# Kernel tuning notes

Measured on AMD Instinct MI355X. Metric: run time of the kernel, lower is better.

## Reference

```python
import jax, jax.numpy as jnp
from jax import lax
import numpy as np

DN = ('NHWC', 'HWIO', 'NHWC')  # NHWC activations, HWIO kernels (TF layout)
EPS = 1e-3


def setup_inputs() -> dict:
    key = jax.random.key(0)
    ks = jax.random.split(key, 6)
    B, H, W, C = 16, 64, 64, 256
    x = jax.random.normal(ks[0], (B, H, W, C), jnp.float32)
    # per-sample predicted kernels (scaled to keep activations well-conditioned)
    depthwise_kernels = jax.random.normal(ks[1], (B, 3, 3, C, C), jnp.float32) * 0.02
    pointwise_kernels = jax.random.normal(ks[2], (B, 1, 1, C, C), jnp.float32) * 0.06
    biases = jax.random.normal(ks[3], (B, C), jnp.float32) * 0.1
    # shared trailing Conv2D layer params
    conv_w = jax.random.normal(ks[4], (3, 3, C, C), jnp.float32) * 0.02
    conv_b = jnp.zeros((C,), jnp.float32)
    return dict(x=x, depthwise_kernels=depthwise_kernels,
                pointwise_kernels=pointwise_kernels, biases=biases,
                conv_w=conv_w, conv_b=conv_b)


def _instance_norm(x):
    # tf.nn.moments over spatial dims (population variance), eps=0.001
    mean = jnp.mean(x, axis=(1, 2), keepdims=True)
    var = jnp.var(x, axis=(1, 2), keepdims=True)
    return (x - mean) * lax.rsqrt(var + EPS)


def _reflect_pad_hw(x, p=1):
    pad = [(0, 0)] * (x.ndim - 3) + [(p, p), (p, p), (0, 0)]
    return jnp.pad(x, pad, mode='reflect')


def _per_sample_conv(xi, dk, pk, bi):
    # xi: [H,W,C]; dk: [3,3,C,Cm]; pk: [1,1,Cm,Co]; bi: [Co]
    xp = _reflect_pad_hw(xi)[None]  # [1,H+2,W+2,C]
    y = lax.conv_general_dilated(xp, dk, (1, 1), 'VALID', dimension_numbers=DN)
    y = lax.conv_general_dilated(y, pk, (1, 1), 'VALID', dimension_numbers=DN)
    return (y + bi)[0]


def reference(x, depthwise_kernels, pointwise_kernels, biases, conv_w, conv_b):
    x = _instance_norm(x)
    # per-sample kernels -> vmap over batch (replaces tf.map_fn)
    x = jax.vmap(_per_sample_conv)(x, depthwise_kernels, pointwise_kernels, biases)
    # shared Conv2D: reflect pad + VALID conv + bias
    xp = _reflect_pad_hw(x)
    y = lax.conv_general_dilated(xp, conv_w, (1, 1), 'VALID', dimension_numbers=DN)
    return y + conv_b
```

## Files before the change

kernel.cpp:

```cpp
#include <hip/hip_runtime.h>


typedef __bf16 bf16x8 __attribute__((ext_vector_type(8)));
typedef float f32x4 __attribute__((ext_vector_type(4)));

__device__ __forceinline__ float bf2f(unsigned short v) {
    return __uint_as_float(((unsigned int)v) << 16);
}
__device__ __forceinline__ unsigned short f2bf(float f) {
    unsigned int u = __float_as_uint(f);
    unsigned int r = (u + 0x7FFFu + ((u >> 16) & 1u)) >> 16;
    return (unsigned short)r;
}
__device__ __forceinline__ float ldg_elem(const void* p, size_t idx, bool isbf) {
    return isbf ? bf2f(((const unsigned short*)p)[idx]) : ((const float*)p)[idx];
}

__device__ __forceinline__ void gload16(const void* g, void* l) {
    __builtin_amdgcn_global_load_lds(
        (__attribute__((address_space(1))) void*)(unsigned long long)g,
        (__attribute__((address_space(3))) void*)(unsigned long long)l,
        16, 0, 0);
}

__global__ void detect_dtype(const unsigned short* __restrict__ x, int* __restrict__ flag) {
    __shared__ int wild;
    if (threadIdx.x == 0) wild = 0;
    __syncthreads();
    int cnt = 0;
    for (int i = 0; i < 16; ++i) {
        float a = fabsf(bf2f(x[threadIdx.x * 16 + i]));
        if (!(a < 64.f) || (a != 0.f && a < 1e-5f)) cnt++;
    }
    atomicAdd(&wild, cnt);
    __syncthreads();
    if (threadIdx.x == 0) *flag = (wild > 512) ? 0 : 1;
}


__global__ void init_stats(float* s) { s[blockIdx.x * 256 + threadIdx.x] = 0.f; }

__global__ void norm_partial(const void* __restrict__ x, const int* __restrict__ flag,
                             float* __restrict__ ssum, float* __restrict__ ssq) {
    const bool isbf = (*flag != 0);
    const int b = blockIdx.x, chunk = blockIdx.y, c = threadIdx.x;
    const size_t base = ((size_t)(b * 4096 + chunk * 64)) * 256 + c;
    float s = 0.f, q = 0.f;
    for (int i = 0; i < 64; ++i) {
        float v = ldg_elem(x, base + (size_t)i * 256, isbf);
        s += v; q += v * v;
    }
    atomicAdd(&ssum[b * 256 + c], s);
    atomicAdd(&ssq[b * 256 + c], q);
}

__global__ void norm_finalize(float* ssum, float* ssq) {
    int i = blockIdx.x * 256 + threadIdx.x;
    float mean = ssum[i] * (1.f / 4096.f);
    float var  = ssq[i]  * (1.f / 4096.f) - mean * mean;
    ssum[i] = mean;
    ssq[i]  = rsqrtf(var + 1e-3f);
}

__global__ void norm_apply(const void* __restrict__ x, const int* __restrict__ flag,
                           const float* __restrict__ mean, const float* __restrict__ rstd,
                           unsigned short* __restrict__ xn) {
    const bool isbf = (*flag != 0);
    size_t e = ((size_t)blockIdx.x * 256 + threadIdx.x) * 8;
    int c0 = (int)(e & 255);
    int bc = (int)(e >> 20) * 256 + c0;
    float v[8];
    if (isbf) {
        uint4 raw = *(const uint4*)((const unsigned short*)x + e);
        unsigned int rr[4] = {raw.x, raw.y, raw.z, raw.w};
#pragma unroll
        for (int i = 0; i < 4; ++i) {
            v[2 * i]     = bf2f((unsigned short)(rr[i] & 0xFFFF));
            v[2 * i + 1] = bf2f((unsigned short)(rr[i] >> 16));
        }
    } else {
        float4 f0 = *(const float4*)((const float*)x + e);
        float4 f1 = *(const float4*)((const float*)x + e + 4);
        v[0] = f0.x; v[1] = f0.y; v[2] = f0.z; v[3] = f0.w;
        v[4] = f1.x; v[5] = f1.y; v[6] = f1.z; v[7] = f1.w;
    }
    unsigned int o[4];
#pragma unroll
    for (int i = 0; i < 4; ++i) {
        unsigned short lo = f2bf((v[2 * i]     - mean[bc + 2 * i])     * rstd[bc + 2 * i]);
        unsigned short hi = f2bf((v[2 * i + 1] - mean[bc + 2 * i + 1]) * rstd[bc + 2 * i + 1]);
        o[i] = (unsigned int)lo | ((unsigned int)hi << 16);
    }
    uint4 out; out.x = o[0]; out.y = o[1]; out.z = o[2]; out.w = o[3];
    *(uint4*)(xn + e) = out;
}

template <bool SCALE>
__global__ void transpose_wk(const void* __restrict__ src, const int* __restrict__ flag,
                             unsigned short* __restrict__ dst,
                             int s_per, long dstBStride, int coStride,
                             const float* __restrict__ rstd) {
    __shared__ unsigned short tile[64][66];
    const bool isbf = (*flag != 0);
    const int sl = blockIdx.x;
    const int b = sl / s_per;
    const size_t dbase = (size_t)b * (size_t)dstBStride + (size_t)(sl % s_per) * 256;
    const int ci0 = blockIdx.y * 64, co0 = blockIdx.z * 64;
    const int t = threadIdx.x;
    const int co4 = (t & 15) * 4;
    const int r0 = t >> 4;
#pragma unroll
    for (int i = 0; i < 4; ++i) {
        int r = r0 + i * 16;
        size_t sidx = (size_t)sl * 65536 + (size_t)(ci0 + r) * 256 + co0 + co4;
        if (isbf) {
            ushort4 v = *(const ushort4*)((const unsigned short*)src + sidx);
            tile[r][co4] = v.x; tile[r][co4 + 1] = v.y;
            tile[r][co4 + 2] = v.z; tile[r][co4 + 3] = v.w;
        } else {
            float4 v = *(const float4*)((const float*)src + sidx);
            tile[r][co4] = f2bf(v.x); tile[r][co4 + 1] = f2bf(v.y);
            tile[r][co4 + 2] = f2bf(v.z); tile[r][co4 + 3] = f2bf(v.w);
        }
    }
    __syncthreads();
    const int cip = (t & 31) * 2;
    const int cob = t >> 5;
    float s0 = 1.f, s1 = 1.f;
    if (SCALE) { s0 = rstd[b * 256 + ci0 + cip]; s1 = rstd[b * 256 + ci0 + cip + 1]; }
#pragma unroll
    for (int i = 0; i < 8; ++i) {
        int co = cob + i * 8;
        unsigned short lo = tile[cip][co], hi = tile[cip + 1][co];
        if (SCALE) { lo = f2bf(bf2f(lo) * s0); hi = f2bf(bf2f(hi) * s1); }
        *(unsigned int*)(dst + dbase + (size_t)(co0 + co) * coStride + ci0 + cip) =
            (unsigned int)lo | ((unsigned int)hi << 16);
    }
}

__global__ void corr_kernel(const unsigned short* __restrict__ dkT,
                            const float* __restrict__ mean,
                            float* __restrict__ negcorr) {
    const int b = blockIdx.x;
    const int lane = threadIdx.x & 63;
    const int co = blockIdx.y * 4 + (threadIdx.x >> 6);
    const unsigned short* wp = dkT + (size_t)(b * 256 + co) * 2304;
    const float* mb = mean + b * 256;
    const int ci0 = (lane & 31) * 8;
    float4 ma = *(const float4*)(mb + ci0);
    float4 mc = *(const float4*)(mb + ci0 + 4);
    float mm[8] = {ma.x, ma.y, ma.z, ma.w, mc.x, mc.y, mc.z, mc.w};
    float sum = 0.f;
#pragma unroll
    for (int c = 0; c < 5; ++c) {
        int k = c * 512 + lane * 8;
        if (k < 2304) {
            uint4 w = *(const uint4*)(wp + k);
            unsigned int wsv[4] = {w.x, w.y, w.z, w.w};
#pragma unroll
            for (int j = 0; j < 4; ++j) {
                sum += bf2f((unsigned short)(wsv[j] & 0xFFFF)) * mm[2 * j];
                sum += bf2f((unsigned short)(wsv[j] >> 16)) * mm[2 * j + 1];
            }
        }
    }
#pragma unroll
    for (int off = 32; off > 0; off >>= 1) sum += __shfl_down(sum, off);
    if (lane == 0) negcorr[b * 256 + co] = -sum;
}

template <int KSLICES, bool PER_SAMPLE_W, int BIAS_MODE, bool IS3X3, bool OUT_F32>
__global__ __launch_bounds__(256) void gemm_conv_dma(const unsigned short* __restrict__ src,
                                                     const int* __restrict__ flag,
                                                     const unsigned short* __restrict__ wT,
                                                     const void* __restrict__ bias,
                                                     void* __restrict__ dst) {
    constexpr int KTOT = KSLICES * 256;
    __shared__ unsigned short As[128 * 64];
    __shared__ unsigned short Bs[128 * 64];

    const int t = threadIdx.x;
    const int lane = t & 63;
    const int wave = t >> 6;
    const int b = blockIdx.z;
    const int m0 = blockIdx.x * 128;
    const int n0 = blockIdx.y * 128;
    const unsigned short* srcB = src + (size_t)b * (4096 * 256);
    const unsigned short* wB = wT + (PER_SAMPLE_W ? (size_t)b * 256 * KTOT : (size_t)0);
    const bool in_bf = (BIAS_MODE >= 2) ? (*flag != 0) : true;

    f32x4 acc[4][4];
#pragma unroll
    for (int i = 0; i < 4; ++i)
#pragma unroll
        for (int j = 0; j < 4; ++j) acc[i][j] = (f32x4){0.f, 0.f, 0.f, 0.f};

    const int lr = lane >> 3;
    const int cidx = lane & 7;
    const int swz = ((cidx ^ lr) << 3);

    int hA[4], wA[4];
    const unsigned short* gB[4];
    unsigned short* ldsA[4];
    unsigned short* ldsB[4];
#pragma unroll
    for (int c = 0; c < 4; ++c) {
        int r = wave * 32 + c * 8;
        int m = m0 + r + lr;
        hA[c] = m >> 6; wA[c] = m & 63;
        gB[c] = wB + (size_t)(n0 + r + lr) * KTOT + swz;
        ldsA[c] = As + r * 64;
        ldsB[c] = Bs + r * 64;
    }

    const int fr = lane & 15;
    const int quad = lane >> 4;
    const int rm = (wave >> 1) * 64;
    const int cn = (wave & 1) * 64;
    const int fsw = fr & 7;

    for (int s = 0; s < KSLICES; ++s) {
        const int dh = IS3X3 ? (s / 3) - 1 : 0;
        const int dw = IS3X3 ? (s % 3) - 1 : 0;
        const unsigned short* gA[4];
#pragma unroll
        for (int c = 0; c < 4; ++c) {
            int hh = hA[c] + dh; hh = (hh < 0) ? 1 : (hh > 63 ? 62 : hh);
            int ww = wA[c] + dw; ww = (ww < 0) ? 1 : (ww > 63 ? 62 : ww);
            gA[c] = srcB + (size_t)((hh << 6) + ww) * 256 + swz;
        }
        const int kbase = s * 256;
#pragma unroll
        for (int cc = 0; cc < 4; ++cc) {
            __syncthreads();
#pragma unroll
            for (int c = 0; c < 4; ++c) {
                gload16(gA[c] + cc * 64, ldsA[c]);
                gload16(gB[c] + kbase + cc * 64, ldsB[c]);
            }
            __syncthreads();

#pragma unroll
            for (int step = 0; step < 2; ++step) {
                const int ks = ((quad + step * 4) ^ fsw) << 3;
                bf16x8 af[4], bfr[4];
#pragma unroll
                for (int i = 0; i < 4; ++i)
                    af[i] = *(const bf16x8*)&As[(rm + i * 16 + fr) * 64 + ks];
#pragma unroll
                for (int j = 0; j < 4; ++j)
                    bfr[j] = *(const bf16x8*)&Bs[(cn + j * 16 + fr) * 64 + ks];
#pragma unroll
                for (int i = 0; i < 4; ++i)
#pragma unroll
                    for (int j = 0; j < 4; ++j)
                        acc[i][j] = __builtin_amdgcn_mfma_f32_16x16x32_bf16(af[i], bfr[j], acc[i][j], 0, 0, 0);
            }
        }
    }

    const int rbase = quad * 4;
    const int col = fr;
    float bv[4];
#pragma unroll
    for (int j = 0; j < 4; ++j) {
        int n = n0 + cn + j * 16 + col;
        if (BIAS_MODE == 2)      bv[j] = ldg_elem(bias, b * 256 + n, in_bf);
        else if (BIAS_MODE == 3) bv[j] = ldg_elem(bias, n, in_bf);
        else                     bv[j] = 0.f;
    }
#pragma unroll
    for (int i = 0; i < 4; ++i) {
#pragma unroll
        for (int rr = 0; rr < 4; ++rr) {
            int m = m0 + rm + i * 16 + rbase + rr;
            size_t rowoff = ((size_t)b * 4096 + m) * 256;
#pragma unroll
            for (int j = 0; j < 4; ++j) {
                int n = n0 + cn + j * 16 + col;
                float val = acc[i][j][rr] + bv[j];
                if (OUT_F32) ((float*)dst)[rowoff + n] = val;
                else         ((unsigned short*)dst)[rowoff + n] = f2bf(val);
            }
        }
    }
}

template <int KSLICES, bool PER_SAMPLE_W, int BIAS_MODE, bool IS3X3, bool SRC_ADAPT, bool OUT_F32>
__global__ __launch_bounds__(256) void gemm_conv(const void* __restrict__ src,
                                                 const int* __restrict__ flag,
                                                 const unsigned short* __restrict__ wT,
                                                 const void* __restrict__ bias,
                                                 void* __restrict__ dst) {
    constexpr int KTOT = KSLICES * 256;
    __shared__ unsigned short As[128][40];
    __shared__ unsigned short Bs[128][40];

    const bool in_bf = (SRC_ADAPT || BIAS_MODE >= 2) ? (*flag != 0) : true;
    const int t = threadIdx.x;
    const int b = blockIdx.z;
    const int m0 = blockIdx.x * 128;
    const int n0 = blockIdx.y * 128;
    const size_t srcOfs = (size_t)b * (4096 * 256);
    const unsigned short* wB = wT + (PER_SAMPLE_W ? (size_t)b * 256 * KTOT : (size_t)0);

    f32x4 acc[4][4];
#pragma unroll
    for (int i = 0; i < 4; ++i)
#pragma unroll
        for (int j = 0; j < 4; ++j) acc[i][j] = (f32x4){0.f, 0.f, 0.f, 0.f};

    const int lane = t & 63;
    const int wave = t >> 6;
    const int rm = (wave >> 1) * 64;
    const int cn = (wave & 1) * 64;
    const int fr = lane & 15;
    const int kg = (lane >> 4) * 8;

    for (int kk = 0; kk < KTOT / 32; ++kk) {
        const int k0 = kk * 32;
        const int s = k0 >> 8;
        const int ci0 = k0 & 255;
        const int dh = IS3X3 ? (s / 3) - 1 : 0;
        const int dw = IS3X3 ? (s % 3) - 1 : 0;
        __syncthreads();
#pragma unroll
        for (int cc = 0; cc < 2; ++cc) {
            int ch = t + cc * 256;
            int r = ch >> 2;
            int ko = (ch & 3) << 3;
            int m = m0 + r;
            int h = m >> 6, w = m & 63;
            if (IS3X3) {
                h += dh; h = (h < 0) ? 1 : (h > 63 ? 62 : h);
                w += dw; w = (w < 0) ? 1 : (w > 63 ? 62 : w);
            }
            size_t eidx = srcOfs + (size_t)((h << 6) + w) * 256 + ci0 + ko;
            if (!SRC_ADAPT || in_bf) {
                uint4 v = *(const uint4*)((const unsigned short*)src + eidx);
                *(uint4*)&As[r][ko] = v;
            } else {
                const float* sf = (const float*)src + eidx;
                float4 f0 = *(const float4*)sf;
                float4 f1 = *(const float4*)(sf + 4);
                uint4 v;
                v.x = (unsigned int)f2bf(f0.x) | ((unsigned int)f2bf(f0.y) << 16);
                v.y = (unsigned int)f2bf(f0.z) | ((unsigned int)f2bf(f0.w) << 16);
                v.z = (unsigned int)f2bf(f1.x) | ((unsigned int)f2bf(f1.y) << 16);
                v.w = (unsigned int)f2bf(f1.z) | ((unsigned int)f2bf(f1.w) << 16);
                *(uint4*)&As[r][ko] = v;
            }
        }
#pragma unroll
        for (int cc = 0; cc < 2; ++cc) {
            int ch = t + cc * 256;
            int n = ch >> 2;
            int ko = (ch & 3) << 3;
            uint4 v = *(const uint4*)(wB + (size_t)(n0 + n) * KTOT + k0 + ko);
            *(uint4*)&Bs[n][ko] = v;
        }
        __syncthreads();

        bf16x8 af[4], bfr[4];
#pragma unroll
        for (int i = 0; i < 4; ++i) af[i] = *(const bf16x8*)&As[rm + i * 16 + fr][kg];
#pragma unroll
        for (int j = 0; j < 4; ++j) bfr[j] = *(const bf16x8*)&Bs[cn + j * 16 + fr][kg];
#pragma unroll
        for (int i = 0; i < 4; ++i)
#pragma unroll
            for (int j = 0; j < 4; ++j)
                acc[i][j] = __builtin_amdgcn_mfma_f32_16x16x32_bf16(af[i], bfr[j], acc[i][j], 0, 0, 0);
    }

    const int rbase = (lane >> 4) * 4;
    const int col = lane & 15;
    float bv[4];
#pragma unroll
    for (int j = 0; j < 4; ++j) {
        int n = n0 + cn + j * 16 + col;
        if (BIAS_MODE == 1)      bv[j] = ((const float*)bias)[b * 256 + n];
        else if (BIAS_MODE == 2) bv[j] = ldg_elem(bias, b * 256 + n, in_bf);
        else if (BIAS_MODE == 3) bv[j] = ldg_elem(bias, n, in_bf);
        else                     bv[j] = 0.f;
    }
#pragma unroll
    for (int i = 0; i < 4; ++i) {
#pragma unroll
        for (int rr = 0; rr < 4; ++rr) {
            int m = m0 + rm + i * 16 + rbase + rr;
            size_t rowoff = ((size_t)b * 4096 + m) * 256;
#pragma unroll
            for (int j = 0; j < 4; ++j) {
                int n = n0 + cn + j * 16 + col;
                float val = acc[i][j][rr] + bv[j];
                if (OUT_F32) ((float*)dst)[rowoff + n] = val;
                else         ((unsigned short*)dst)[rowoff + n] = f2bf(val);
            }
        }
    }
}

extern "C" void kernel_launch(void* const* d_in, const int* in_sizes, int n_in,
                              void* d_out, int out_size, void* d_ws, size_t ws_size,
                              hipStream_t stream) {
    const void* x    = d_in[0];
    const void* dk   = d_in[1];
    const void* pk   = d_in[2];
    const void* bias = d_in[3];
    const void* cw   = d_in[4];
    const void* cb   = d_in[5];

    const size_t NEED_SMALL = 36896768u;
    const size_t NEED_BIG   = 55771136u;
    if (ws_size < NEED_SMALL) return;
    const bool big = (ws_size >= NEED_BIG);

    char* ws = (char*)d_ws;
    int*   flagp   = (int*)ws;
    float* meanp   = (float*)(ws + 1024);
    float* rstdp   = (float*)(ws + 17408);
    float* negcorr = (float*)(ws + 33792);
    unsigned short* pkT = (unsigned short*)(ws + 65536);
    unsigned short* cwT = (unsigned short*)(ws + 2162688);
    unsigned short* dkT = (unsigned short*)(ws + 3342336);
    unsigned short* xn  = (unsigned short*)(ws + 22216704);
    unsigned short* y2  = big ? xn : dkT;
    unsigned short* y1  = (unsigned short*)d_out;

    detect_dtype<<<1, 256, 0, stream>>>((const unsigned short*)x, flagp);
    init_stats<<<32, 256, 0, stream>>>(meanp);
    norm_partial<<<dim3(16, 64), 256, 0, stream>>>(x, flagp, meanp, rstdp);
    norm_finalize<<<16, 256, 0, stream>>>(meanp, rstdp);

    transpose_wk<false><<<dim3(16, 4, 4), 256, 0, stream>>>(pk, flagp, pkT, 1, 65536L, 256, nullptr);
    transpose_wk<false><<<dim3(9, 4, 4), 256, 0, stream>>>(cw, flagp, cwT, 9, 0L, 2304, nullptr);

    if (big) {
        transpose_wk<false><<<dim3(144, 4, 4), 256, 0, stream>>>(dk, flagp, dkT, 9, 589824L, 2304, nullptr);
        norm_apply<<<8192, 256, 0, stream>>>(x, flagp, meanp, rstdp, xn);
        gemm_conv_dma<9, true, 0, true, false><<<dim3(32, 2, 16), 256, 0, stream>>>(xn, flagp, dkT, nullptr, y1);
    } else {
        transpose_wk<true><<<dim3(144, 4, 4), 256, 0, stream>>>(dk, flagp, dkT, 9, 589824L, 2304, rstdp);
        corr_kernel<<<dim3(16, 64), 256, 0, stream>>>(dkT, meanp, negcorr);
        gemm_conv<9, true, 1, true, true, false><<<dim3(32, 2, 16), 256, 0, stream>>>(x, flagp, dkT, negcorr, y1);
    }

    gemm_conv_dma<1, true, 2, false, false><<<dim3(32, 2, 16), 256, 0, stream>>>(y1, flagp, pkT, bias, y2);
    gemm_conv_dma<9, false, 3, true, true><<<dim3(32, 2, 16), 256, 0, stream>>>(y2, flagp, cwT, cb, d_out);
}
```

Before: 390.1 us.

## Add 256x256-tile 512-thread pipelined GEMM for the 3x3 convolutions

```diff
diff --git a/kernel.cpp b/kernel.cpp
--- a/kernel.cpp
+++ b/kernel.cpp
@@ -22,6 +22,10 @@
         (__attribute__((address_space(3))) void*)(unsigned long long)l,
         16, 0, 0);
 }
+
+#define RAW_BARRIER() do { asm volatile("" ::: "memory"); \
+                           __builtin_amdgcn_s_barrier();   \
+                           asm volatile("" ::: "memory"); } while (0)
 
 __global__ void detect_dtype(const unsigned short* __restrict__ x, int* __restrict__ flag) {
     __shared__ int wild;
@@ -170,6 +174,204 @@
 }
 
 template <int KSLICES, bool PER_SAMPLE_W, int BIAS_MODE, bool IS3X3, bool OUT_F32>
+__global__ __launch_bounds__(512, 2) void gemm_conv_256(const unsigned short* __restrict__ src,
+                                                        const int* __restrict__ flag,
+                                                        const unsigned short* __restrict__ wT,
+                                                        const void* __restrict__ bias,
+                                                        void* __restrict__ dst) {
+    constexpr int KTOT = KSLICES * 256;
+    constexpr int NKT = KTOT / 64;
+    static_assert(NKT >= 2, "pipeline needs >=2 K-tiles");
+    extern __shared__ unsigned short smem[];
+
+    const int t = threadIdx.x;
+    const int lane = t & 63;
+    const int wave = t >> 6;
+    const int wr = wave >> 2;
+    const int wc = wave & 3;
+    const int b = blockIdx.z;
+    const int m0 = blockIdx.x * 256;
+    const unsigned short* srcB = src + (size_t)b * (4096 * 256);
+    const unsigned short* wB = wT + (PER_SAMPLE_W ? (size_t)b * 256 * KTOT : (size_t)0);
+    const bool in_bf = (BIAS_MODE >= 2) ? (*flag != 0) : true;
+
+    const int trow = t >> 3;
+    const int tswz = ((t & 7) ^ (trow & 7)) << 3;
+    int hU[4], wU[4];
+#pragma unroll
+    for (int u = 0; u < 4; ++u) {
+        int m = m0 + u * 64 + trow;
+        hU[u] = m >> 6; wU[u] = m & 63;
+    }
+    const unsigned short* gBu[4];
+#pragma unroll
+    for (int u = 0; u < 4; ++u)
+        gBu[u] = wB + (size_t)(u * 64 + trow) * KTOT + tswz;
+
+    f32x4 acc[8][4];
+#pragma unroll
+    for (int i = 0; i < 8; ++i)
+#pragma unroll
+        for (int j = 0; j < 4; ++j) acc[i][j] = (f32x4){0.f, 0.f, 0.f, 0.f};
+
+    const int fr = lane & 15;
+    const int quad = lane >> 4;
+    const int fsw = fr & 7;
+    const int ks0 = ((quad) ^ fsw) << 3;
+    const int ks1 = ((quad + 4) ^ fsw) << 3;
+    const int rm = wr * 128;
+    const int cn = wc * 64;
+
+#pragma unroll
+    for (int kt = 0; kt < 2; ++kt) {
+        const int s0_ = kt >> 2;
+        const int pdh = IS3X3 ? (s0_ / 3) - 1 : 0;
+        const int pdw = IS3X3 ? (s0_ % 3) - 1 : 0;
+        const int pchb = (kt & 3) << 6;
+        unsigned short* ldsAW = smem + kt * 32768 + wave * 512;
+#pragma unroll
+        for (int u = 0; u < 4; ++u) {
+            int hh = hU[u] + pdh; hh = (hh < 0) ? 1 : (hh > 63 ? 62 : hh);
+            int ww = wU[u] + pdw; ww = (ww < 0) ? 1 : (ww > 63 ? 62 : ww);
+            gload16(srcB + (size_t)((hh << 6) + ww) * 256 + pchb + tswz, ldsAW + u * 4096);
+        }
+#pragma unroll
+        for (int u = 0; u < 4; ++u)
+            gload16(gBu[u] + (size_t)kt * 64, ldsAW + 16384 + u * 4096);
+    }
+    asm volatile("s_waitcnt vmcnt(8)" ::: "memory");
+    RAW_BARRIER();
+
+    bf16x8 af[4][2], bfr[4][2];
+
+    for (int i = 0; i < NKT; ++i) {
+        const int buf = i & 1;
+        const unsigned short* As_b = smem + buf * 32768;
+        const unsigned short* Bs_b = As_b + 16384;
+        unsigned short* ldsAW = smem + buf * 32768 + wave * 512;
+        const int kt2 = i + 2;
+        const bool st = (kt2 < NKT);
+        int dh2 = 0, dw2 = 0, chb2 = 0;
+        if (st) {
+            int s2 = kt2 >> 2;
+            dh2 = IS3X3 ? (s2 / 3) - 1 : 0;
+            dw2 = IS3X3 ? (s2 % 3) - 1 : 0;
+            chb2 = (kt2 & 3) << 6;
+        }
+        auto stA = [&](int u) {
+            int hh = hU[u] + dh2; hh = (hh < 0) ? 1 : (hh > 63 ? 62 : hh);
+            int ww = wU[u] + dw2; ww = (ww < 0) ? 1 : (ww > 63 ? 62 : ww);
+            gload16(srcB + (size_t)((hh << 6) + ww) * 256 + chb2 + tswz, ldsAW + u * 4096);
+        };
+        auto stB = [&](int u) {
+            gload16(gBu[u] + (size_t)kt2 * 64, ldsAW + 16384 + u * 4096);
+        };
+
+#pragma unroll
+        for (int m = 0; m < 4; ++m) {
+            const unsigned short* rp = As_b + (rm + m * 16 + fr) * 64;
+            af[m][0] = *(const bf16x8*)(rp + ks0);
+            af[m][1] = *(const bf16x8*)(rp + ks1);
+        }
+#pragma unroll
+        for (int n = 0; n < 2; ++n) {
+            const unsigned short* rp = Bs_b + (cn + n * 16 + fr) * 64;
+            bfr[n][0] = *(const bf16x8*)(rp + ks0);
+            bfr[n][1] = *(const bf16x8*)(rp + ks1);
+        }
+        RAW_BARRIER();
+        __builtin_amdgcn_s_setprio(1);
+#pragma unroll
+        for (int m = 0; m < 4; ++m)
+#pragma unroll
+            for (int n = 0; n < 2; ++n) {
+                acc[m][n] = __builtin_amdgcn_mfma_f32_16x16x32_bf16(af[m][0], bfr[n][0], acc[m][n], 0, 0, 0);
+                acc[m][n] = __builtin_amdgcn_mfma_f32_16x16x32_bf16(af[m][1], bfr[n][1], acc[m][n], 0, 0, 0);
+            }
+        __builtin_amdgcn_s_setprio(0);
+        RAW_BARRIER();
+
+#pragma unroll
+        for (int n = 2; n < 4; ++n) {
+            const unsigned short* rp = Bs_b + (cn + n * 16 + fr) * 64;
+            bfr[n][0] = *(const bf16x8*)(rp + ks0);
+            bfr[n][1] = *(const bf16x8*)(rp + ks1);
+        }
+        if (st) { stA(0); stA(2); }
+        RAW_BARRIER();
+        __builtin_amdgcn_s_setprio(1);
+#pragma unroll
+        for (int m = 0; m < 4; ++m)
+#pragma unroll
+            for (int n = 2; n < 4; ++n) {
+                acc[m][n] = __builtin_amdgcn_mfma_f32_16x16x32_bf16(af[m][0], bfr[n][0], acc[m][n], 0, 0, 0);
+                acc[m][n] = __builtin_amdgcn_mfma_f32_16x16x32_bf16(af[m][1], bfr[n][1], acc[m][n], 0, 0, 0);
+            }
+        __builtin_amdgcn_s_setprio(0);
+        RAW_BARRIER();
+
+#pragma unroll
+        for (int m = 0; m < 4; ++m) {
+            const unsigned short* rp = As_b + (rm + 64 + m * 16 + fr) * 64;
+            af[m][0] = *(const bf16x8*)(rp + ks0);
+            af[m][1] = *(const bf16x8*)(rp + ks1);
+        }
+        if (st) { stB(0); stB(1); }
+        RAW_BARRIER();
+        __builtin_amdgcn_s_setprio(1);
+#pragma unroll
+        for (int m = 0; m < 4; ++m)
+#pragma unroll
+            for (int n = 0; n < 2; ++n) {
+                acc[4 + m][n] = __builtin_amdgcn_mfma_f32_16x16x32_bf16(af[m][0], bfr[n][0], acc[4 + m][n], 0, 0, 0);
+                acc[4 + m][n] = __builtin_amdgcn_mfma_f32_16x16x32_bf16(af[m][1], bfr[n][1], acc[4 + m][n], 0, 0, 0);
+            }
+        __builtin_amdgcn_s_setprio(0);
+        RAW_BARRIER();
+
+        if (st) { stB(2); stB(3); stA(1); stA(3); }
+        RAW_BARRIER();
+        __builtin_amdgcn_s_setprio(1);
+#pragma unroll
+        for (int m = 0; m < 4; ++m)
+#pragma unroll
+            for (int n = 2; n < 4; ++n) {
+                acc[4 + m][n] = __builtin_amdgcn_mfma_f32_16x16x32_bf16(af[m][0], bfr[n][0], acc[4 + m][n], 0, 0, 0);
+                acc[4 + m][n] = __builtin_amdgcn_mfma_f32_16x16x32_bf16(af[m][1], bfr[n][1], acc[4 + m][n], 0, 0, 0);
+            }
+        __builtin_amdgcn_s_setprio(0);
+        if (st)                  asm volatile("s_waitcnt vmcnt(8)" ::: "memory");
+        else if (i + 1 < NKT)    asm volatile("s_waitcnt vmcnt(0)" ::: "memory");
+        RAW_BARRIER();
+    }
+
+    const int rbase = quad * 4;
+    float bv[4];
+#pragma unroll
+    for (int n = 0; n < 4; ++n) {
+        int nn = cn + n * 16 + fr;
+        if (BIAS_MODE == 2)      bv[n] = ldg_elem(bias, b * 256 + nn, in_bf);
+        else if (BIAS_MODE == 3) bv[n] = ldg_elem(bias, nn, in_bf);
+        else                     bv[n] = 0.f;
+    }
+#pragma unroll
+    for (int m = 0; m < 8; ++m) {
+#pragma unroll
+        for (int rr = 0; rr < 4; ++rr) {
+            int mm = m0 + rm + m * 16 + rbase + rr;
+            size_t rowoff = ((size_t)b * 4096 + mm) * 256;
+#pragma unroll
+            for (int n = 0; n < 4; ++n) {
+                int nn = cn + n * 16 + fr;
+                float val = acc[m][n][rr] + bv[n];
+                if (OUT_F32) ((float*)dst)[rowoff + nn] = val;
+                else         ((unsigned short*)dst)[rowoff + nn] = f2bf(val);
+            }
+        }
+    }
+}
+
+template <int KSLICES, bool PER_SAMPLE_W, int BIAS_MODE, bool IS3X3, bool OUT_F32>
 __global__ __launch_bounds__(256) void gemm_conv_dma(const unsigned short* __restrict__ src,
                                                      const int* __restrict__ flag,
                                                      const unsigned short* __restrict__ wT,
@@ -428,6 +630,11 @@
     unsigned short* y2  = big ? xn : dkT;
     unsigned short* y1  = (unsigned short*)d_out;
 
+    hipFuncSetAttribute(reinterpret_cast<const void*>(gemm_conv_256<9, true, 0, true, false>),
+                        hipFuncAttributeMaxDynamicSharedMemorySize, 131072);
+    hipFuncSetAttribute(reinterpret_cast<const void*>(gemm_conv_256<9, false, 3, true, true>),
+                        hipFuncAttributeMaxDynamicSharedMemorySize, 131072);
+
     detect_dtype<<<1, 256, 0, stream>>>((const unsigned short*)x, flagp);
     init_stats<<<32, 256, 0, stream>>>(meanp);
     norm_partial<<<dim3(16, 64), 256, 0, stream>>>(x, flagp, meanp, rstdp);
@@ -439,7 +646,7 @@
     if (big) {
         transpose_wk<false><<<dim3(144, 4, 4), 256, 0, stream>>>(dk, flagp, dkT, 9, 589824L, 2304, nullptr);
         norm_apply<<<8192, 256, 0, stream>>>(x, flagp, meanp, rstdp, xn);
-        gemm_conv_dma<9, true, 0, true, false><<<dim3(32, 2, 16), 256, 0, stream>>>(xn, flagp, dkT, nullptr, y1);
+        gemm_conv_256<9, true, 0, true, false><<<dim3(16, 1, 16), 512, 131072, stream>>>(xn, flagp, dkT, nullptr, y1);
     } else {
         transpose_wk<true><<<dim3(144, 4, 4), 256, 0, stream>>>(dk, flagp, dkT, 9, 589824L, 2304, rstdp);
         corr_kernel<<<dim3(16, 64), 256, 0, stream>>>(dkT, meanp, negcorr);
@@ -447,5 +654,5 @@
     }
 
     gemm_conv_dma<1, true, 2, false, false><<<dim3(32, 2, 16), 256, 0, stream>>>(y1, flagp, pkT, bias, y2);
-    gemm_conv_dma<9, false, 3, true, true><<<dim3(32, 2, 16), 256, 0, stream>>>(y2, flagp, cwT, cb, d_out);
-}
+    gemm_conv_256<9, false, 3, true, true><<<dim3(16, 1, 16), 512, 131072, stream>>>(y2, flagp, cwT, cb, d_out);
+}
```

Measured after the change: 378.4 us. 3.0% less time.
